# Kernel optimization log

Hardware: AMD Instinct MI355X
Metric: run time of the kernel (lower is better)

The kernel has to match this reference:

```python
import jax, jax.numpy as jnp
import numpy as np
import math

NUM_HEADS = 16
THETA = 10000.0


def _rope(x, token_pos, theta):
    # x: [B, H, S, d_k]; token_pos: [S]
    d_k = x.shape[-1]
    freqs = 1.0 / theta ** (jnp.arange(0, d_k, 2, dtype=jnp.float32) / d_k)  # [d_k/2]
    angles = token_pos.astype(jnp.float32)[:, None] * freqs[None, :]         # [S, d_k/2]
    cos, sin = jnp.cos(angles), jnp.sin(angles)
    x1 = x[..., 0::2]
    x2 = x[..., 1::2]
    out1 = x1 * cos - x2 * sin
    out2 = x1 * sin + x2 * cos
    # interleave back: (..., d_k/2, 2) -> (..., d_k)
    return jnp.stack([out1, out2], axis=-1).reshape(x.shape)


def setup_inputs() -> dict:
    key = jax.random.key(0)
    ks = jax.random.split(key, 5)
    B, S, D = 4, 2048, 1024
    scale = 0.02
    return {
        "x": jax.random.normal(ks[0], (B, S, D), dtype=jnp.float32),
        "token_pos": jnp.arange(S, dtype=jnp.int64 if jax.config.jax_enable_x64 else jnp.int32),
        "Wq": jax.random.normal(ks[1], (D, D), dtype=jnp.float32) * scale,
        "Wk": jax.random.normal(ks[2], (D, D), dtype=jnp.float32) * scale,
        "Wv": jax.random.normal(ks[3], (D, D), dtype=jnp.float32) * scale,
        "Wo": jax.random.normal(ks[4], (D, D), dtype=jnp.float32) * scale,
    }


def reference(x, token_pos, Wq, Wk, Wv, Wo):
    B, S, D = x.shape
    H = NUM_HEADS
    d_k = D // H
    # projections (Linear without bias: y = x @ W^T, W is [out, in])
    def proj(W):
        y = jnp.einsum('bsd,ed->bse', x, W)
        return y.reshape(B, S, H, d_k).transpose(0, 2, 1, 3)  # [B,H,S,d_k]
    q, k, v = proj(Wq), proj(Wk), proj(Wv)
    q = _rope(q, token_pos, THETA)
    k = _rope(k, token_pos, THETA)
    scores = jnp.einsum('bhqd,bhkd->bhqk', q, k) / math.sqrt(d_k)
    causal = jnp.tril(jnp.ones((S, S), dtype=bool))
    scores = jnp.where(causal, scores, -jnp.inf)
    attn = jax.nn.softmax(scores, axis=-1)
    out = jnp.einsum('bhqk,bhkd->bhqd', attn, v)            # [B,H,S,d_k]
    out = out.transpose(0, 2, 1, 3).reshape(B, S, D)
    return jnp.einsum('bsd,ed->bse', out, Wo)
```

## Files before the change

kernel.cpp:

```cpp
#include <hip/hip_runtime.h>

typedef unsigned short u16;
typedef __bf16 bf16x8 __attribute__((ext_vector_type(8)));
typedef float f32x4 __attribute__((ext_vector_type(4)));
typedef u16 u16x8 __attribute__((ext_vector_type(8)));

#define B_ 4
#define S_ 2048
#define D_ 1024
#define H_ 16
#define LOG2E 1.44269504f

__device__ inline u16 f2bf(float f) {
  unsigned u = __float_as_uint(f);
  u = u + 0x7fffu + ((u >> 16) & 1u);
  return (u16)(u >> 16);
}
__device__ inline u16 f2bf_hw(float f) {
  __bf16 b = (__bf16)f;
  return __builtin_bit_cast(u16, b);
}
__device__ inline float bf2f(u16 h) {
  return __uint_as_float(((unsigned)h) << 16);
}
__device__ inline void gload_lds16(const u16* g, u16* l) {
  __builtin_amdgcn_global_load_lds((const __attribute__((address_space(1))) void*)g,
                                   (__attribute__((address_space(3))) void*)l, 16, 0, 0);
}

__global__ __launch_bounds__(256) void k_f32_to_bf16(const float* __restrict__ src,
                                                     u16* __restrict__ dst, int n4) {
  int i = blockIdx.x * 256 + threadIdx.x;
  if (i >= n4) return;
  float4 v = reinterpret_cast<const float4*>(src)[i];
  ushort4 o;
  o.x = f2bf(v.x); o.y = f2bf(v.y); o.z = f2bf(v.z); o.w = f2bf(v.w);
  reinterpret_cast<ushort4*>(dst)[i] = o;
}

__global__ __launch_bounds__(256) void k_cvt_w4(const float* __restrict__ w0,
                                                const float* __restrict__ w1,
                                                const float* __restrict__ w2,
                                                const float* __restrict__ w3,
                                                u16* __restrict__ dst) {
  int i = blockIdx.x * 256 + threadIdx.x;
  const int tensor = i >> 18;
  const int local = i & 262143;
  const float* s = tensor == 0 ? w0 : tensor == 1 ? w1 : tensor == 2 ? w2 : w3;
  float4 v = reinterpret_cast<const float4*>(s)[local];
  ushort4 o;
  o.x = f2bf(v.x); o.y = f2bf(v.y); o.z = f2bf(v.z); o.w = f2bf(v.w);
  reinterpret_cast<ushort4*>(dst + (size_t)tensor * 1048576)[local] = o;
}

__global__ __launch_bounds__(256) void k_rope_table(const int* __restrict__ pos,
                                                    float2* __restrict__ tab) {
  int idx = blockIdx.x * 256 + threadIdx.x;
  if (idx >= S_ * 32) return;
  int s = idx >> 5, i = idx & 31;
  float freq = powf(10000.0f, -(float)i * (1.0f / 32.0f));
  float ang = (float)pos[s] * freq;
  float sn, c;
  sincosf(ang, &sn, &c);
  tab[idx] = make_float2(c, sn);
}

__global__ __launch_bounds__(256) void k_rope_k(u16* __restrict__ kb,
                                                const float2* __restrict__ tab) {
  int idx = blockIdx.x * 256 + threadIdx.x;
  const int row = idx >> 7;
  const int s = row & 2047;
  const int chunk = idx & 127;
  u16* p = kb + ((size_t)row << 10) + chunk * 8;
  u16x8 v = *reinterpret_cast<u16x8*>(p);
  const float4* tp = reinterpret_cast<const float4*>(tab + s * 32 + (chunk & 7) * 4);
  float4 t0 = tp[0], t1 = tp[1];
  float cc[4] = {t0.x, t0.z, t1.x, t1.z};
  float ss[4] = {t0.y, t0.w, t1.y, t1.w};
  u16x8 o;
#pragma unroll
  for (int u = 0; u < 4; u++) {
    float x1 = bf2f(v[2 * u]), x2 = bf2f(v[2 * u + 1]);
    o[2 * u]     = f2bf(x1 * cc[u] - x2 * ss[u]);
    o[2 * u + 1] = f2bf(x1 * ss[u] + x2 * cc[u]);
  }
  *reinterpret_cast<u16x8*>(p) = o;
}

__global__ __launch_bounds__(256) void k_gemm_qkv(const u16* __restrict__ A,
                                                  const u16* __restrict__ Bcat,
                                                  u16* __restrict__ Ccat) {
  __shared__ u16 As[128 * 32];
  __shared__ u16 Bs[128 * 32];
  const int K = 1024;
  const int swz = (blockIdx.x & 7) * 192 + (blockIdx.x >> 3);
  const int bx = swz % 24;
  const int by = swz / 24;
  const int m0 = by << 7, n0 = bx << 7;
  const int tid = threadIdx.x;
  const int lane = tid & 63;
  const int wv = tid >> 6;
  const int wm = (wv >> 1) << 6;
  const int wn = (wv & 1) << 6;
  const int r = lane & 15, g = lane >> 4;

  f32x4 acc[4][4] = {};

  const int o0 = tid << 4;
  const int o1 = o0 + 4096;
  const int am0 = o0 >> 6, ak0 = (o0 & 63) >> 1;
  const int am1 = o1 >> 6, ak1 = (o1 & 63) >> 1;

  for (int k0 = 0; k0 < K; k0 += 32) {
    gload_lds16(A + (size_t)(m0 + am0) * K + k0 + ak0, As + (o0 >> 1));
    gload_lds16(A + (size_t)(m0 + am1) * K + k0 + ak1, As + (o1 >> 1));
    gload_lds16(Bcat + (size_t)(n0 + am0) * K + k0 + ak0, Bs + (o0 >> 1));
    gload_lds16(Bcat + (size_t)(n0 + am1) * K + k0 + ak1, Bs + (o1 >> 1));
    __syncthreads();
    bf16x8 af[4], bfr[4];
#pragma unroll
    for (int i = 0; i < 4; i++)
      af[i] = *reinterpret_cast<const bf16x8*>(&As[(wm + i * 16 + r) * 32 + g * 8]);
#pragma unroll
    for (int t = 0; t < 4; t++)
      bfr[t] = *reinterpret_cast<const bf16x8*>(&Bs[(wn + t * 16 + r) * 32 + g * 8]);
#pragma unroll
    for (int i = 0; i < 4; i++)
#pragma unroll
      for (int t = 0; t < 4; t++)
        acc[i][t] = __builtin_amdgcn_mfma_f32_16x16x32_bf16(af[i], bfr[t], acc[i][t], 0, 0, 0);
    __syncthreads();
  }

  u16* Cb = Ccat + (size_t)(n0 >> 10) * (8192 * 1024);
  const int c0 = n0 & 1023;
#pragma unroll
  for (int i = 0; i < 4; i++) {
#pragma unroll
    for (int t = 0; t < 4; t++) {
      const int row = m0 + wm + i * 16 + g * 4;
      const int col = c0 + wn + t * 16 + r;
#pragma unroll
      for (int j = 0; j < 4; j++)
        Cb[(size_t)(row + j) * 1024 + col] = f2bf(acc[i][t][j]);
    }
  }
}

__global__ __launch_bounds__(256) void k_gemm_bt(const u16* __restrict__ A,
                                                 const u16* __restrict__ Bw,
                                                 float* __restrict__ C,
                                                 int M, int N, int K) {
  __shared__ u16 As[128 * 32];
  __shared__ u16 Bs[128 * 32];
  const int nbx = N >> 7;
  const int swz = (blockIdx.x & 7) * (gridDim.x >> 3) + (blockIdx.x >> 3);
  const int bx = swz % nbx;
  const int by = swz / nbx;
  const int m0 = by << 7, n0 = bx << 7;
  const int tid = threadIdx.x;
  const int lane = tid & 63;
  const int wv = tid >> 6;
  const int wm = (wv >> 1) << 6;
  const int wn = (wv & 1) << 6;
  const int r = lane & 15, g = lane >> 4;

  f32x4 acc[4][4] = {};

  const int o0 = tid << 4;
  const int o1 = o0 + 4096;
  const int am0 = o0 >> 6, ak0 = (o0 & 63) >> 1;
  const int am1 = o1 >> 6, ak1 = (o1 & 63) >> 1;

  for (int k0 = 0; k0 < K; k0 += 32) {
    gload_lds16(A + (size_t)(m0 + am0) * K + k0 + ak0, As + (o0 >> 1));
    gload_lds16(A + (size_t)(m0 + am1) * K + k0 + ak1, As + (o1 >> 1));
    gload_lds16(Bw + (size_t)(n0 + am0) * K + k0 + ak0, Bs + (o0 >> 1));
    gload_lds16(Bw + (size_t)(n0 + am1) * K + k0 + ak1, Bs + (o1 >> 1));
    __syncthreads();
    bf16x8 af[4], bfr[4];
#pragma unroll
    for (int i = 0; i < 4; i++)
      af[i] = *reinterpret_cast<const bf16x8*>(&As[(wm + i * 16 + r) * 32 + g * 8]);
#pragma unroll
    for (int t = 0; t < 4; t++)
      bfr[t] = *reinterpret_cast<const bf16x8*>(&Bs[(wn + t * 16 + r) * 32 + g * 8]);
#pragma unroll
    for (int i = 0; i < 4; i++)
#pragma unroll
      for (int t = 0; t < 4; t++)
        acc[i][t] = __builtin_amdgcn_mfma_f32_16x16x32_bf16(af[i], bfr[t], acc[i][t], 0, 0, 0);
    __syncthreads();
  }

#pragma unroll
  for (int i = 0; i < 4; i++) {
#pragma unroll
    for (int t = 0; t < 4; t++) {
      const int row = m0 + wm + i * 16 + g * 4;
      const int col = n0 + wn + t * 16 + r;
#pragma unroll
      for (int j = 0; j < 4; j++)
        C[(size_t)(row + j) * N + col] = acc[i][t][j];
    }
  }
}

__global__ __launch_bounds__(256) void k_transpose_v(const u16* __restrict__ Vb,
                                                     u16* __restrict__ Vt) {
  __shared__ u16 tile[64][65];
  int bh = blockIdx.x >> 5;
  int st = blockIdx.x & 31;
  int b = bh >> 4, h = bh & 15;
  int s0 = st << 6;
  int tid = threadIdx.x;
#pragma unroll
  for (int rr = 0; rr < 16; rr++) {
    int idx = rr * 256 + tid;
    int sl = idx >> 6, d = idx & 63;
    tile[d][sl] = Vb[(size_t)(b * S_ + s0 + sl) * 1024 + h * 64 + d];
  }
  __syncthreads();
#pragma unroll
  for (int rr = 0; rr < 16; rr++) {
    int idx = rr * 256 + tid;
    int d = idx >> 6, sl = idx & 63;
    Vt[(size_t)(bh * 64 + d) * 2048 + s0 + sl] = tile[d][sl];
  }
}

__global__ __launch_bounds__(256) void k_attn9(const u16* __restrict__ Q,
                                               const u16* __restrict__ Kb,
                                               const u16* __restrict__ Vt,
                                               const float2* __restrict__ tab,
                                               u16* __restrict__ O) {
  __shared__ u16 Ks[64 * 64];
  __shared__ u16 Vs[64 * 64];
  __shared__ u16 Ps[4][32 * 64];

  const int bh = (blockIdx.x & 7) * 8 + ((blockIdx.x >> 3) & 7);
  const int qt = 15 - (blockIdx.x >> 6);
  const int b = bh >> 4, h = bh & 15;
  const int tid = threadIdx.x;
  const int lane = tid & 63, w = tid >> 6;
  const int g = lane >> 4, r = lane & 15;

  const u16* Kbase = Kb + (size_t)(b * S_) * 1024 + h * 64;
  const u16* Vbase = Vt + (size_t)bh * 64 * 2048;

  const int srow = tid >> 3;
  const int scol = ((tid & 7) * 8) ^ ((srow & 7) * 8);
  const int rsw = (r & 7) * 8;

  const int qbase = qt << 7;
  const int qrow0 = qbase + (w << 5);

  const float QSC = 0.125f * LOG2E;
  bf16x8 qf[2][2];
#pragma unroll
  for (int f = 0; f < 2; f++) {
    const int s = qrow0 + f * 16 + r;
    const u16* qrow = Q + (size_t)(b * S_ + s) * 1024 + h * 64;
    qf[f][0] = *reinterpret_cast<const bf16x8*>(qrow + g * 8);
    qf[f][1] = *reinterpret_cast<const bf16x8*>(qrow + 32 + g * 8);
    const float4* tp = reinterpret_cast<const float4*>(tab + s * 32);
#pragma unroll
    for (int c = 0; c < 2; c++) {
      float4 t0 = tp[c * 8 + g * 2], t1 = tp[c * 8 + g * 2 + 1];
      float cc[4] = {t0.x, t0.z, t1.x, t1.z};
      float ss[4] = {t0.y, t0.w, t1.y, t1.w};
      bf16x8 q = qf[f][c];
#pragma unroll
      for (int u = 0; u < 4; u++) {
        float x1 = (float)q[2 * u], x2 = (float)q[2 * u + 1];
        q[2 * u]     = (__bf16)((x1 * cc[u] - x2 * ss[u]) * QSC);
        q[2 * u + 1] = (__bf16)((x1 * ss[u] + x2 * cc[u]) * QSC);
      }
      qf[f][c] = q;
    }
  }

  f32x4 o_acc[2][4] = {};
  float l0 = 0.f, l1 = 0.f;
  u16* pb0 = &Ps[w][r * 64];
  u16* pb1 = &Ps[w][(16 + r) * 64];

  const int kend = qbase + 128;
  for (int k0 = 0; k0 < kend; k0 += 64) {
    gload_lds16(Kbase + (size_t)(k0 + srow) * 1024 + scol, Ks + tid * 8);
    gload_lds16(Kbase + (size_t)(k0 + srow + 32) * 1024 + scol, Ks + tid * 8 + 2048);
    gload_lds16(Vbase + (size_t)srow * 2048 + k0 + scol, Vs + tid * 8);
    gload_lds16(Vbase + (size_t)(srow + 32) * 2048 + k0 + scol, Vs + tid * 8 + 2048);
    __syncthreads();

    if (k0 <= qrow0 + 31) {
      const int rem0 = qrow0 + 15 - k0;
      const int rem1 = qrow0 + 31 - k0;
      const int ktlim0 = rem0 < 0 ? 0 : (rem0 >= 48 ? 4 : (rem0 >> 4) + 1);
      const int ktlim1 = rem1 >= 48 ? 4 : (rem1 >> 4) + 1;
      const bool mask0 = (k0 + 63 > qrow0);
      const bool mask1 = (k0 + 63 > qrow0 + 16);

#pragma unroll
      for (int kt = 0; kt < 4; kt++) {
        const int pc = (kt * 16 + g * 4) ^ rsw;
        if (kt >= ktlim1) {
          ushort4 z = {0, 0, 0, 0};
          *reinterpret_cast<ushort4*>(pb0 + pc) = z;
          *reinterpret_cast<ushort4*>(pb1 + pc) = z;
          continue;
        }
        const int krow = kt * 16 + r;
        bf16x8 kf0 = *reinterpret_cast<const bf16x8*>(&Ks[krow * 64 + ((g * 8) ^ rsw)]);
        bf16x8 kf1 = *reinterpret_cast<const bf16x8*>(&Ks[krow * 64 + ((32 + g * 8) ^ rsw)]);
        f32x4 s0 = {}, s1 = {};
        __builtin_amdgcn_s_setprio(1);
        if (kt < ktlim0) {
          s0 = __builtin_amdgcn_mfma_f32_16x16x32_bf16(kf0, qf[0][0], s0, 0, 0, 0);
          s0 = __builtin_amdgcn_mfma_f32_16x16x32_bf16(kf1, qf[0][1], s0, 0, 0, 0);
        }
        s1 = __builtin_amdgcn_mfma_f32_16x16x32_bf16(kf0, qf[1][0], s1, 0, 0, 0);
        s1 = __builtin_amdgcn_mfma_f32_16x16x32_bf16(kf1, qf[1][1], s1, 0, 0, 0);
        __builtin_amdgcn_s_setprio(0);

        const int colb = k0 + kt * 16 + g * 4;
        float p0[4], p1[4];
        if (kt < ktlim0) {
          if (mask0) {
#pragma unroll
            for (int j = 0; j < 4; j++)
              if (colb + j > qrow0 + r) s0[j] = -1e30f;
          }
#pragma unroll
          for (int j = 0; j < 4; j++) p0[j] = exp2f(s0[j]);
          l0 += (p0[0] + p0[1]) + (p0[2] + p0[3]);
        } else {
#pragma unroll
          for (int j = 0; j < 4; j++) p0[j] = 0.f;
        }
        if (mask1) {
#pragma unroll
          for (int j = 0; j < 4; j++)
            if (colb + j > qrow0 + 16 + r) s1[j] = -1e30f;
        }
#pragma unroll
        for (int j = 0; j < 4; j++) p1[j] = exp2f(s1[j]);
        l1 += (p1[0] + p1[1]) + (p1[2] + p1[3]);

        ushort4 w0, w1;
        w0.x = f2bf_hw(p0[0]); w0.y = f2bf_hw(p0[1]); w0.z = f2bf_hw(p0[2]); w0.w = f2bf_hw(p0[3]);
        w1.x = f2bf_hw(p1[0]); w1.y = f2bf_hw(p1[1]); w1.z = f2bf_hw(p1[2]); w1.w = f2bf_hw(p1[3]);
        *reinterpret_cast<ushort4*>(pb0 + pc) = w0;
        *reinterpret_cast<ushort4*>(pb1 + pc) = w1;
      }
      asm volatile("s_waitcnt lgkmcnt(0)" ::: "memory");

      __builtin_amdgcn_s_setprio(1);
#pragma unroll
      for (int kc = 0; kc < 2; kc++) {
        const int cb = (kc * 32 + g * 8) ^ rsw;
        bf16x8 pf0 = *reinterpret_cast<const bf16x8*>(pb0 + cb);
        bf16x8 pf1 = *reinterpret_cast<const bf16x8*>(pb1 + cb);
#pragma unroll
        for (int dt = 0; dt < 4; dt++) {
          bf16x8 vf = *reinterpret_cast<const bf16x8*>(
              &Vs[(dt * 16 + r) * 64 + ((kc * 32 + g * 8) ^ rsw)]);
          o_acc[0][dt] = __builtin_amdgcn_mfma_f32_16x16x32_bf16(pf0, vf, o_acc[0][dt], 0, 0, 0);
          o_acc[1][dt] = __builtin_amdgcn_mfma_f32_16x16x32_bf16(pf1, vf, o_acc[1][dt], 0, 0, 0);
        }
      }
      __builtin_amdgcn_s_setprio(0);
    }
    __syncthreads();
  }

  l0 += __shfl_xor(l0, 16); l0 += __shfl_xor(l0, 32);
  l1 += __shfl_xor(l1, 16); l1 += __shfl_xor(l1, 32);

#pragma unroll
  for (int f = 0; f < 2; f++) {
    u16* orow = O + (size_t)(b * S_ + qrow0 + f * 16) * 1024 + h * 64;
#pragma unroll
    for (int j = 0; j < 4; j++) {
      const float ln = __shfl(f ? l1 : l0, 4 * g + j);
      const float rln = 1.0f / ln;
#pragma unroll
      for (int dt = 0; dt < 4; dt++)
        orow[(size_t)(g * 4 + j) * 1024 + dt * 16 + r] = f2bf(o_acc[f][dt][j] * rln);
    }
  }
}

extern "C" void kernel_launch(void* const* d_in, const int* in_sizes, int n_in,
                              void* d_out, int out_size, void* d_ws, size_t ws_size,
                              hipStream_t stream) {
  const float* x  = (const float*)d_in[0];
  const int*   pos = (const int*)d_in[1];
  const float* Wq = (const float*)d_in[2];
  const float* Wk = (const float*)d_in[3];
  const float* Wv = (const float*)d_in[4];
  const float* Wo = (const float*)d_in[5];
  float* out = (float*)d_out;

  char* ws = (char*)d_ws;
  size_t off = 0;
  auto alloc = [&](size_t bytes) {
    void* p = ws + off;
    off += (bytes + 255) & ~(size_t)255;
    return p;
  };
  const size_t XB = (size_t)8192 * 1024 * 2;
  u16* xb  = (u16*)alloc(XB);
  u16* wqb = (u16*)alloc((size_t)1024 * 1024 * 2);
  u16* wkb = (u16*)alloc((size_t)1024 * 1024 * 2);
  u16* wvb = (u16*)alloc((size_t)1024 * 1024 * 2);
  u16* wob = (u16*)alloc((size_t)1024 * 1024 * 2);
  u16* qb  = (u16*)alloc(XB);
  u16* kb  = (u16*)alloc(XB);
  u16* vb  = (u16*)alloc(XB);
  u16* vt  = (u16*)alloc(XB);
  float2* tab = (float2*)alloc((size_t)2048 * 32 * sizeof(float2));
  u16* ob = vb;
  (void)wkb; (void)wvb;

  k_f32_to_bf16<<<8192, 256, 0, stream>>>(x, xb, 2097152);
  k_cvt_w4<<<4096, 256, 0, stream>>>(Wq, Wk, Wv, Wo, wqb);
  k_rope_table<<<256, 256, 0, stream>>>(pos, tab);

  k_gemm_qkv<<<1536, 256, 0, stream>>>(xb, wqb, qb);

  k_rope_k<<<4096, 256, 0, stream>>>(kb, tab);

  k_transpose_v<<<2048, 256, 0, stream>>>(vb, vt);

  k_attn9<<<1024, 256, 0, stream>>>(qb, kb, vt, tab, ob);

  k_gemm_bt<<<512, 256, 0, stream>>>(ob, wob, out, 8192, 1024, 1024);
}
```

Before: 204.0 us.

## Fuse V transpose into QKV GEMM epilogue and pair causal q-tiles per block

The QKV GEMM epilogue now writes the V projection directly in transposed [b,h,d,s] layout, which removes the separate transpose kernel and its extra round trip through global memory. The attention kernel runs half as many blocks, and each block handles two query tiles, qp and 15-qp, so every block gets the same causal work and the tail imbalance shrinks. The s_setprio hints are dropped. The transposed V stores are 4-element writes with a large stride, so they may coalesce poorly, and with 512 blocks each block runs longer and occupancy changes.

```diff
diff --git a/kernel.cpp b/kernel.cpp
--- a/kernel.cpp
+++ b/kernel.cpp
@@ -89,7 +89,8 @@
 
 __global__ __launch_bounds__(256) void k_gemm_qkv(const u16* __restrict__ A,
                                                   const u16* __restrict__ Bcat,
-                                                  u16* __restrict__ Ccat) {
+                                                  u16* __restrict__ Ccat,
+                                                  u16* __restrict__ Vt) {
   __shared__ u16 As[128 * 32];
   __shared__ u16 Bs[128 * 32];
   const int K = 1024;
@@ -132,17 +133,36 @@
     __syncthreads();
   }
 
-  u16* Cb = Ccat + (size_t)(n0 >> 10) * (8192 * 1024);
+  const int bq = n0 >> 10;
   const int c0 = n0 & 1023;
-#pragma unroll
-  for (int i = 0; i < 4; i++) {
-#pragma unroll
-    for (int t = 0; t < 4; t++) {
-      const int row = m0 + wm + i * 16 + g * 4;
-      const int col = c0 + wn + t * 16 + r;
-#pragma unroll
-      for (int j = 0; j < 4; j++)
-        Cb[(size_t)(row + j) * 1024 + col] = f2bf(acc[i][t][j]);
+  if (bq == 2) {
+#pragma unroll
+    for (int i = 0; i < 4; i++) {
+#pragma unroll
+      for (int t = 0; t < 4; t++) {
+        const int row = m0 + wm + i * 16 + g * 4;
+        const int col = c0 + wn + t * 16 + r;
+        const int b = row >> 11, s0 = row & 2047;
+        const int h = col >> 6, d = col & 63;
+        ushort4 o;
+        o.x = f2bf(acc[i][t][0]); o.y = f2bf(acc[i][t][1]);
+        o.z = f2bf(acc[i][t][2]); o.w = f2bf(acc[i][t][3]);
+        *reinterpret_cast<ushort4*>(
+            Vt + (((size_t)(b * 16 + h) * 64 + d) << 11) + s0) = o;
+      }
+    }
+  } else {
+    u16* Cb = Ccat + (size_t)bq * (8192 * 1024);
+#pragma unroll
+    for (int i = 0; i < 4; i++) {
+#pragma unroll
+      for (int t = 0; t < 4; t++) {
+        const int row = m0 + wm + i * 16 + g * 4;
+        const int col = c0 + wn + t * 16 + r;
+#pragma unroll
+        for (int j = 0; j < 4; j++)
+          Cb[(size_t)(row + j) * 1024 + col] = f2bf(acc[i][t][j]);
+      }
     }
   }
 }
@@ -206,40 +226,17 @@
   }
 }
 
-__global__ __launch_bounds__(256) void k_transpose_v(const u16* __restrict__ Vb,
-                                                     u16* __restrict__ Vt) {
-  __shared__ u16 tile[64][65];
-  int bh = blockIdx.x >> 5;
-  int st = blockIdx.x & 31;
-  int b = bh >> 4, h = bh & 15;
-  int s0 = st << 6;
-  int tid = threadIdx.x;
-#pragma unroll
-  for (int rr = 0; rr < 16; rr++) {
-    int idx = rr * 256 + tid;
-    int sl = idx >> 6, d = idx & 63;
-    tile[d][sl] = Vb[(size_t)(b * S_ + s0 + sl) * 1024 + h * 64 + d];
-  }
-  __syncthreads();
-#pragma unroll
-  for (int rr = 0; rr < 16; rr++) {
-    int idx = rr * 256 + tid;
-    int d = idx >> 6, sl = idx & 63;
-    Vt[(size_t)(bh * 64 + d) * 2048 + s0 + sl] = tile[d][sl];
-  }
-}
-
-__global__ __launch_bounds__(256) void k_attn9(const u16* __restrict__ Q,
-                                               const u16* __restrict__ Kb,
-                                               const u16* __restrict__ Vt,
-                                               const float2* __restrict__ tab,
-                                               u16* __restrict__ O) {
+__global__ __launch_bounds__(256) void k_attn10(const u16* __restrict__ Q,
+                                                const u16* __restrict__ Kb,
+                                                const u16* __restrict__ Vt,
+                                                const float2* __restrict__ tab,
+                                                u16* __restrict__ O) {
   __shared__ u16 Ks[64 * 64];
   __shared__ u16 Vs[64 * 64];
   __shared__ u16 Ps[4][32 * 64];
 
   const int bh = (blockIdx.x & 7) * 8 + ((blockIdx.x >> 3) & 7);
-  const int qt = 15 - (blockIdx.x >> 6);
+  const int qp = blockIdx.x >> 6;
   const int b = bh >> 4, h = bh & 15;
   const int tid = threadIdx.x;
   const int lane = tid & 63, w = tid >> 6;
@@ -252,141 +249,141 @@
   const int scol = ((tid & 7) * 8) ^ ((srow & 7) * 8);
   const int rsw = (r & 7) * 8;
 
-  const int qbase = qt << 7;
-  const int qrow0 = qbase + (w << 5);
-
-  const float QSC = 0.125f * LOG2E;
-  bf16x8 qf[2][2];
-#pragma unroll
-  for (int f = 0; f < 2; f++) {
-    const int s = qrow0 + f * 16 + r;
-    const u16* qrow = Q + (size_t)(b * S_ + s) * 1024 + h * 64;
-    qf[f][0] = *reinterpret_cast<const bf16x8*>(qrow + g * 8);
-    qf[f][1] = *reinterpret_cast<const bf16x8*>(qrow + 32 + g * 8);
-    const float4* tp = reinterpret_cast<const float4*>(tab + s * 32);
-#pragma unroll
-    for (int c = 0; c < 2; c++) {
-      float4 t0 = tp[c * 8 + g * 2], t1 = tp[c * 8 + g * 2 + 1];
-      float cc[4] = {t0.x, t0.z, t1.x, t1.z};
-      float ss[4] = {t0.y, t0.w, t1.y, t1.w};
-      bf16x8 q = qf[f][c];
-#pragma unroll
-      for (int u = 0; u < 4; u++) {
-        float x1 = (float)q[2 * u], x2 = (float)q[2 * u + 1];
-        q[2 * u]     = (__bf16)((x1 * cc[u] - x2 * ss[u]) * QSC);
-        q[2 * u + 1] = (__bf16)((x1 * ss[u] + x2 * cc[u]) * QSC);
-      }
-      qf[f][c] = q;
-    }
-  }
-
-  f32x4 o_acc[2][4] = {};
-  float l0 = 0.f, l1 = 0.f;
   u16* pb0 = &Ps[w][r * 64];
   u16* pb1 = &Ps[w][(16 + r) * 64];
-
-  const int kend = qbase + 128;
-  for (int k0 = 0; k0 < kend; k0 += 64) {
-    gload_lds16(Kbase + (size_t)(k0 + srow) * 1024 + scol, Ks + tid * 8);
-    gload_lds16(Kbase + (size_t)(k0 + srow + 32) * 1024 + scol, Ks + tid * 8 + 2048);
-    gload_lds16(Vbase + (size_t)srow * 2048 + k0 + scol, Vs + tid * 8);
-    gload_lds16(Vbase + (size_t)(srow + 32) * 2048 + k0 + scol, Vs + tid * 8 + 2048);
-    __syncthreads();
-
-    if (k0 <= qrow0 + 31) {
-      const int rem0 = qrow0 + 15 - k0;
-      const int rem1 = qrow0 + 31 - k0;
-      const int ktlim0 = rem0 < 0 ? 0 : (rem0 >= 48 ? 4 : (rem0 >> 4) + 1);
-      const int ktlim1 = rem1 >= 48 ? 4 : (rem1 >> 4) + 1;
-      const bool mask0 = (k0 + 63 > qrow0);
-      const bool mask1 = (k0 + 63 > qrow0 + 16);
-
-#pragma unroll
-      for (int kt = 0; kt < 4; kt++) {
-        const int pc = (kt * 16 + g * 4) ^ rsw;
-        if (kt >= ktlim1) {
-          ushort4 z = {0, 0, 0, 0};
-          *reinterpret_cast<ushort4*>(pb0 + pc) = z;
-          *reinterpret_cast<ushort4*>(pb1 + pc) = z;
-          continue;
+  const float QSC = 0.125f * LOG2E;
+
+  for (int ph = 0; ph < 2; ph++) {
+    const int qt = ph ? (15 - qp) : qp;
+    const int qbase = qt << 7;
+    const int qrow0 = qbase + (w << 5);
+
+    bf16x8 qf[2][2];
+#pragma unroll
+    for (int f = 0; f < 2; f++) {
+      const int s = qrow0 + f * 16 + r;
+      const u16* qrow = Q + (size_t)(b * S_ + s) * 1024 + h * 64;
+      qf[f][0] = *reinterpret_cast<const bf16x8*>(qrow + g * 8);
+      qf[f][1] = *reinterpret_cast<const bf16x8*>(qrow + 32 + g * 8);
+      const float4* tp = reinterpret_cast<const float4*>(tab + s * 32);
+#pragma unroll
+      for (int c = 0; c < 2; c++) {
+        float4 t0 = tp[c * 8 + g * 2], t1 = tp[c * 8 + g * 2 + 1];
+        float cc[4] = {t0.x, t0.z, t1.x, t1.z};
+        float ss[4] = {t0.y, t0.w, t1.y, t1.w};
+        bf16x8 q = qf[f][c];
+#pragma unroll
+        for (int u = 0; u < 4; u++) {
+          float x1 = (float)q[2 * u], x2 = (float)q[2 * u + 1];
+          q[2 * u]     = (__bf16)((x1 * cc[u] - x2 * ss[u]) * QSC);
+          q[2 * u + 1] = (__bf16)((x1 * ss[u] + x2 * cc[u]) * QSC);
         }
-        const int krow = kt * 16 + r;
-        bf16x8 kf0 = *reinterpret_cast<const bf16x8*>(&Ks[krow * 64 + ((g * 8) ^ rsw)]);
-        bf16x8 kf1 = *reinterpret_cast<const bf16x8*>(&Ks[krow * 64 + ((32 + g * 8) ^ rsw)]);
-        f32x4 s0 = {}, s1 = {};
-        __builtin_amdgcn_s_setprio(1);
-        if (kt < ktlim0) {
-          s0 = __builtin_amdgcn_mfma_f32_16x16x32_bf16(kf0, qf[0][0], s0, 0, 0, 0);
-          s0 = __builtin_amdgcn_mfma_f32_16x16x32_bf16(kf1, qf[0][1], s0, 0, 0, 0);
+        qf[f][c] = q;
+      }
+    }
+
+    f32x4 o_acc[2][4] = {};
+    float l0 = 0.f, l1 = 0.f;
+
+    const int kend = qbase + 128;
+    for (int k0 = 0; k0 < kend; k0 += 64) {
+      gload_lds16(Kbase + (size_t)(k0 + srow) * 1024 + scol, Ks + tid * 8);
+      gload_lds16(Kbase + (size_t)(k0 + srow + 32) * 1024 + scol, Ks + tid * 8 + 2048);
+      gload_lds16(Vbase + (size_t)srow * 2048 + k0 + scol, Vs + tid * 8);
+      gload_lds16(Vbase + (size_t)(srow + 32) * 2048 + k0 + scol, Vs + tid * 8 + 2048);
+      __syncthreads();
+
+      if (k0 <= qrow0 + 31) {
+        const int rem0 = qrow0 + 15 - k0;
+        const int rem1 = qrow0 + 31 - k0;
+        const int ktlim0 = rem0 < 0 ? 0 : (rem0 >= 48 ? 4 : (rem0 >> 4) + 1);
+        const int ktlim1 = rem1 >= 48 ? 4 : (rem1 >> 4) + 1;
+        const bool mask0 = (k0 + 63 > qrow0);
+        const bool mask1 = (k0 + 63 > qrow0 + 16);
+
+#pragma unroll
+        for (int kt = 0; kt < 4; kt++) {
+          const int pc = (kt * 16 + g * 4) ^ rsw;
+          if (kt >= ktlim1) {
+            ushort4 z = {0, 0, 0, 0};
+            *reinterpret_cast<ushort4*>(pb0 + pc) = z;
+            *reinterpret_cast<ushort4*>(pb1 + pc) = z;
+            continue;
+          }
+          const int krow = kt * 16 + r;
+          bf16x8 kf0 = *reinterpret_cast<const bf16x8*>(&Ks[krow * 64 + ((g * 8) ^ rsw)]);
+          bf16x8 kf1 = *reinterpret_cast<const bf16x8*>(&Ks[krow * 64 + ((32 + g * 8) ^ rsw)]);
+          f32x4 s0 = {}, s1 = {};
+          if (kt < ktlim0) {
+            s0 = __builtin_amdgcn_mfma_f32_16x16x32_bf16(kf0, qf[0][0], s0, 0, 0, 0);
+            s0 = __builtin_amdgcn_mfma_f32_16x16x32_bf16(kf1, qf[0][1], s0, 0, 0, 0);
+          }
+          s1 = __builtin_amdgcn_mfma_f32_16x16x32_bf16(kf0, qf[1][0], s1, 0, 0, 0);
+          s1 = __builtin_amdgcn_mfma_f32_16x16x32_bf16(kf1, qf[1][1], s1, 0, 0, 0);
+
+          const int colb = k0 + kt * 16 + g * 4;
+          float p0[4], p1[4];
+          if (kt < ktlim0) {
+            if (mask0) {
+#pragma unroll
+              for (int j = 0; j < 4; j++)
+                if (colb + j > qrow0 + r) s0[j] = -1e30f;
+            }
+#pragma unroll
+            for (int j = 0; j < 4; j++) p0[j] = exp2f(s0[j]);
+            l0 += (p0[0] + p0[1]) + (p0[2] + p0[3]);
+          } else {
+#pragma unroll
+            for (int j = 0; j < 4; j++) p0[j] = 0.f;
+          }
+          if (mask1) {
+#pragma unroll
+            for (int j = 0; j < 4; j++)
+              if (colb + j > qrow0 + 16 + r) s1[j] = -1e30f;
+          }
+#pragma unroll
+          for (int j = 0; j < 4; j++) p1[j] = exp2f(s1[j]);
+          l1 += (p1[0] + p1[1]) + (p1[2] + p1[3]);
+
+          ushort4 w0, w1;
+          w0.x = f2bf_hw(p0[0]); w0.y = f2bf_hw(p0[1]); w0.z = f2bf_hw(p0[2]); w0.w = f2bf_hw(p0[3]);
+          w1.x = f2bf_hw(p1[0]); w1.y = f2bf_hw(p1[1]); w1.z = f2bf_hw(p1[2]); w1.w = f2bf_hw(p1[3]);
+          *reinterpret_cast<ushort4*>(pb0 + pc) = w0;
+          *reinterpret_cast<ushort4*>(pb1 + pc) = w1;
         }
-        s1 = __builtin_amdgcn_mfma_f32_16x16x32_bf16(kf0, qf[1][0], s1, 0, 0, 0);
-        s1 = __builtin_amdgcn_mfma_f32_16x16x32_bf16(kf1, qf[1][1], s1, 0, 0, 0);
-        __builtin_amdgcn_s_setprio(0);
-
-        const int colb = k0 + kt * 16 + g * 4;
-        float p0[4], p1[4];
-        if (kt < ktlim0) {
-          if (mask0) {
-#pragma unroll
-            for (int j = 0; j < 4; j++)
-              if (colb + j > qrow0 + r) s0[j] = -1e30f;
+        asm volatile("s_waitcnt lgkmcnt(0)" ::: "memory");
+
+#pragma unroll
+        for (int kc = 0; kc < 2; kc++) {
+          const int cb = (kc * 32 + g * 8) ^ rsw;
+          bf16x8 pf0 = *reinterpret_cast<const bf16x8*>(pb0 + cb);
+          bf16x8 pf1 = *reinterpret_cast<const bf16x8*>(pb1 + cb);
+#pragma unroll
+          for (int dt = 0; dt < 4; dt++) {
+            bf16x8 vf = *reinterpret_cast<const bf16x8*>(
+                &Vs[(dt * 16 + r) * 64 + ((kc * 32 + g * 8) ^ rsw)]);
+            o_acc[0][dt] = __builtin_amdgcn_mfma_f32_16x16x32_bf16(pf0, vf, o_acc[0][dt], 0, 0, 0);
+            o_acc[1][dt] = __builtin_amdgcn_mfma_f32_16x16x32_bf16(pf1, vf, o_acc[1][dt], 0, 0, 0);
           }
-#pragma unroll
-          for (int j = 0; j < 4; j++) p0[j] = exp2f(s0[j]);
-          l0 += (p0[0] + p0[1]) + (p0[2] + p0[3]);
-        } else {
-#pragma unroll
-          for (int j = 0; j < 4; j++) p0[j] = 0.f;
-        }
-        if (mask1) {
-#pragma unroll
-          for (int j = 0; j < 4; j++)
-            if (colb + j > qrow0 + 16 + r) s1[j] = -1e30f;
-        }
-#pragma unroll
-        for (int j = 0; j < 4; j++) p1[j] = exp2f(s1[j]);
-        l1 += (p1[0] + p1[1]) + (p1[2] + p1[3]);
-
-        ushort4 w0, w1;
-        w0.x = f2bf_hw(p0[0]); w0.y = f2bf_hw(p0[1]); w0.z = f2bf_hw(p0[2]); w0.w = f2bf_hw(p0[3]);
-        w1.x = f2bf_hw(p1[0]); w1.y = f2bf_hw(p1[1]); w1.z = f2bf_hw(p1[2]); w1.w = f2bf_hw(p1[3]);
-        *reinterpret_cast<ushort4*>(pb0 + pc) = w0;
-        *reinterpret_cast<ushort4*>(pb1 + pc) = w1;
-      }
-      asm volatile("s_waitcnt lgkmcnt(0)" ::: "memory");
-
-      __builtin_amdgcn_s_setprio(1);
-#pragma unroll
-      for (int kc = 0; kc < 2; kc++) {
-        const int cb = (kc * 32 + g * 8) ^ rsw;
-        bf16x8 pf0 = *reinterpret_cast<const bf16x8*>(pb0 + cb);
-        bf16x8 pf1 = *reinterpret_cast<const bf16x8*>(pb1 + cb);
-#pragma unroll
-        for (int dt = 0; dt < 4; dt++) {
-          bf16x8 vf = *reinterpret_cast<const bf16x8*>(
-              &Vs[(dt * 16 + r) * 64 + ((kc * 32 + g * 8) ^ rsw)]);
-          o_acc[0][dt] = __builtin_amdgcn_mfma_f32_16x16x32_bf16(pf0, vf, o_acc[0][dt], 0, 0, 0);
-          o_acc[1][dt] = __builtin_amdgcn_mfma_f32_16x16x32_bf16(pf1, vf, o_acc[1][dt], 0, 0, 0);
         }
       }
-      __builtin_amdgcn_s_setprio(0);
-    }
-    __syncthreads();
-  }
-
-  l0 += __shfl_xor(l0, 16); l0 += __shfl_xor(l0, 32);
-  l1 += __shfl_xor(l1, 16); l1 += __shfl_xor(l1, 32);
-
-#pragma unroll
-  for (int f = 0; f < 2; f++) {
-    u16* orow = O + (size_t)(b * S_ + qrow0 + f * 16) * 1024 + h * 64;
-#pragma unroll
-    for (int j = 0; j < 4; j++) {
-      const float ln = __shfl(f ? l1 : l0, 4 * g + j);
-      const float rln = 1.0f / ln;
-#pragma unroll
-      for (int dt = 0; dt < 4; dt++)
-        orow[(size_t)(g * 4 + j) * 1024 + dt * 16 + r] = f2bf(o_acc[f][dt][j] * rln);
+      __syncthreads();
+    }
+
+    l0 += __shfl_xor(l0, 16); l0 += __shfl_xor(l0, 32);
+    l1 += __shfl_xor(l1, 16); l1 += __shfl_xor(l1, 32);
+
+#pragma unroll
+    for (int f = 0; f < 2; f++) {
+      u16* orow = O + (size_t)(b * S_ + qrow0 + f * 16) * 1024 + h * 64;
+#pragma unroll
+      for (int j = 0; j < 4; j++) {
+        const float ln = __shfl(f ? l1 : l0, 4 * g + j);
+        const float rln = 1.0f / ln;
+#pragma unroll
+        for (int dt = 0; dt < 4; dt++)
+          orow[(size_t)(g * 4 + j) * 1024 + dt * 16 + r] = f2bf(o_acc[f][dt][j] * rln);
+      }
     }
   }
 }
@@ -417,23 +414,20 @@
   u16* wob = (u16*)alloc((size_t)1024 * 1024 * 2);
   u16* qb  = (u16*)alloc(XB);
   u16* kb  = (u16*)alloc(XB);
-  u16* vb  = (u16*)alloc(XB);
+  u16* ob  = (u16*)alloc(XB);
   u16* vt  = (u16*)alloc(XB);
   float2* tab = (float2*)alloc((size_t)2048 * 32 * sizeof(float2));
-  u16* ob = vb;
   (void)wkb; (void)wvb;
 
   k_f32_to_bf16<<<8192, 256, 0, stream>>>(x, xb, 2097152);
   k_cvt_w4<<<4096, 256, 0, stream>>>(Wq, Wk, Wv, Wo, wqb);
   k_rope_table<<<256, 256, 0, stream>>>(pos, tab);
 
-  k_gemm_qkv<<<1536, 256, 0, stream>>>(xb, wqb, qb);
+  k_gemm_qkv<<<1536, 256, 0, stream>>>(xb, wqb, qb, vt);
 
   k_rope_k<<<4096, 256, 0, stream>>>(kb, tab);
 
-  k_transpose_v<<<2048, 256, 0, stream>>>(vb, vt);
-
-  k_attn9<<<1024, 256, 0, stream>>>(qb, kb, vt, tab, ob);
+  k_attn10<<<512, 256, 0, stream>>>(qb, kb, vt, tab, ob);
 
   k_gemm_bt<<<512, 256, 0, stream>>>(ob, wob, out, 8192, 1024, 1024);
 }
```

Result: slower. 223.1 us (+9.4%).
